# Kernel tuning notes

Measured on AMD Instinct MI355X. Metric: run time of the kernel, lower is better.

## Reference

```python
import jax, jax.numpy as jnp
import numpy as np

V, H, B, S = 32000, 2048, 128, 512
NEG_INF = -1e9

def setup_inputs() -> dict:
    key = jax.random.key(0)
    ks = jax.random.split(key, 12)
    sc = 1.0 / np.sqrt(H)
    embed = jax.random.normal(ks[0], (V, H), jnp.float32) * sc
    embed = embed.at[0].set(0.0)  # padding_idx=0
    return {
        "target_words": jax.random.randint(ks[1], (B,), 0, V),
        "hx": jax.random.normal(ks[2], (B, H), jnp.float32),
        "cx": jax.random.normal(ks[3], (B, H), jnp.float32),
        "ew_hx_list": jax.random.normal(ks[4], (S, B, H), jnp.float32),
        "ew_mask": jax.random.randint(ks[5], (S, B, 1), 0, 2).astype(jnp.int32),
        "embed": embed,
        "W_ih": jax.random.normal(ks[6], (4 * H, H), jnp.float32) * sc,
        "W_hh": jax.random.normal(ks[7], (4 * H, H), jnp.float32) * sc,
        "b_ih": jax.random.normal(ks[8], (4 * H,), jnp.float32) * sc,
        "b_hh": jax.random.normal(ks[9], (4 * H,), jnp.float32) * sc,
        "attn_W": jax.random.normal(ks[10], (H, 2 * H), jnp.float32) * sc,
        "attn_b": jax.random.normal(ks[11], (H,), jnp.float32) * sc,
    }

def reference(target_words, hx, cx, ew_hx_list, ew_mask, embed, W_ih, W_hh, b_ih, b_hh, attn_W, attn_b):
    # forward(): embedding (dropout is identity in eval) + LSTMCell step
    x = embed[target_words]                                   # [B,H]
    gates = x @ W_ih.T + b_ih + hx @ W_hh.T + b_hh            # [B,4H]
    i, f, g, o = jnp.split(gates, 4, axis=-1)                 # PyTorch gate order
    i = jax.nn.sigmoid(i); f = jax.nn.sigmoid(f); o = jax.nn.sigmoid(o)
    g = jnp.tanh(g)
    cx_new = f * cx + i * g
    hx_new = o * jnp.tanh(cx_new)                             # [B,H]
    # attention(): masked dot-score softmax over source dim 0
    scores = jnp.sum(hx_new * ew_hx_list, axis=-1, keepdims=True)  # [S,B,1]
    masked = jnp.where(ew_mask == 0, NEG_INF, scores)
    align = jax.nn.softmax(masked, axis=0)                    # [S,B,1]
    content = jnp.sum(align * ew_hx_list, axis=0)             # [B,H]
    concat = jnp.concatenate([content, hx_new], axis=1)       # [B,2H]
    hx_attention = jnp.tanh(concat @ attn_W.T + attn_b)       # [B,H]
    return hx_attention
```

## Files before the change

kernel.cpp:

```cpp
#include <hip/hip_runtime.h>
#include <math.h>

#define B 128
#define H 2048
#define S 512
#define FOURH 8192

typedef float  f32x4  __attribute__((ext_vector_type(4)));
typedef short  bf16x8 __attribute__((ext_vector_type(8)));
typedef unsigned short u16;
typedef unsigned short u16x8 __attribute__((ext_vector_type(8)));
typedef unsigned short u16x4 __attribute__((ext_vector_type(4)));

__device__ __forceinline__ void cvt_hilo(float x, u16& h, u16& lo) {
    unsigned int u = __float_as_uint(x);
    h = (u16)(u >> 16);
    float hf = __uint_as_float(u & 0xFFFF0000u);
    float r = x - hf;
    lo = (u16)(__float_as_uint(r) >> 16);
}

__global__ __launch_bounds__(256) void gather_convert_A0(
    const int* __restrict__ tw,
    const float* __restrict__ embed,
    const float* __restrict__ hx,
    u16* __restrict__ Ah, u16* __restrict__ Al)
{
    const int i = (blockIdx.x * 256 + threadIdx.x) * 8;
    const int b = i >> 12;
    const int col = i & 4095;
    const float* src = (col < H) ? (embed + (size_t)tw[b] * H + col)
                                 : (hx + (size_t)b * H + (col - H));
    f32x4 v0 = *(const f32x4*)(src);
    f32x4 v1 = *(const f32x4*)(src + 4);
    u16x8 hv, lv;
    #pragma unroll
    for (int j = 0; j < 4; ++j) { u16 h, l; cvt_hilo(v0[j], h, l); hv[j] = h; lv[j] = l; }
    #pragma unroll
    for (int j = 0; j < 4; ++j) { u16 h, l; cvt_hilo(v1[j], h, l); hv[4+j] = h; lv[4+j] = l; }
    *(u16x8*)(Ah + i) = hv;
    *(u16x8*)(Al + i) = lv;
}

template<int MODE>
__global__ __launch_bounds__(256) void split_gemm(
    const u16* __restrict__ Ah, const u16* __restrict__ Al,
    const float* __restrict__ W0, const float* __restrict__ W1,
    float* __restrict__ outp)
{
    constexpr int NOUT = (MODE == 0) ? FOURH : H;
    constexpr int KLEN = (MODE == 0) ? 2048 : 1024;
    __shared__ u16 AhS[128][40];
    __shared__ u16 AlS[128][40];
    __shared__ u16 BhS[32][40];
    __shared__ u16 BlS[32][40];

    const int tid = threadIdx.x;
    const int n0 = blockIdx.x * 32;
    const int kz = blockIdx.y;
    const int kbase = kz * KLEN;
    const int ar = tid >> 1, ac = (tid & 1) * 16;
    const int br = tid >> 3, bc = (tid & 7) * 4;
    const int wv = tid >> 6, lane = tid & 63;
    const int frow = lane & 15, fk = (lane >> 4) * 8, crow = (lane >> 4) * 4;

    const float* Wrow;
    if (MODE == 0)
        Wrow = ((kz == 0) ? W0 : W1) + (size_t)(n0 + br) * H;
    else
        Wrow = W0 + (size_t)(n0 + br) * (2 * H) + kbase;

    const u16* Abase = Ah + (size_t)ar * 4096 + kbase + ac;
    const u16* Lbase = Al + (size_t)ar * 4096 + kbase + ac;

    f32x4 acc[2][2];
    #pragma unroll
    for (int mi = 0; mi < 2; ++mi)
        #pragma unroll
        for (int ni = 0; ni < 2; ++ni)
            acc[mi][ni] = (f32x4){0.f, 0.f, 0.f, 0.f};

    u16x8 rah0, rah1, ral0, ral1;
    f32x4 rbv;
    auto load_tile = [&](int k0) {
        rah0 = *(const u16x8*)(Abase + k0);
        rah1 = *(const u16x8*)(Abase + k0 + 8);
        ral0 = *(const u16x8*)(Lbase + k0);
        ral1 = *(const u16x8*)(Lbase + k0 + 8);
        rbv  = *(const f32x4*)(Wrow + k0 + bc);
    };

    load_tile(0);

    for (int ks = 0; ks < KLEN / 32; ++ks) {
        __syncthreads();
        *(u16x8*)&AhS[ar][ac]     = rah0;
        *(u16x8*)&AhS[ar][ac + 8] = rah1;
        *(u16x8*)&AlS[ar][ac]     = ral0;
        *(u16x8*)&AlS[ar][ac + 8] = ral1;
        u16x4 bh, bl;
        #pragma unroll
        for (int j = 0; j < 4; ++j) { u16 h, l; cvt_hilo(rbv[j], h, l); bh[j] = h; bl[j] = l; }
        *(u16x4*)&BhS[br][bc] = bh;
        *(u16x4*)&BlS[br][bc] = bl;
        __syncthreads();
        if (ks + 1 < KLEN / 32) load_tile((ks + 1) * 32);

        bf16x8 a_h[2], a_l[2], b_h[2], b_l[2];
        #pragma unroll
        for (int mi = 0; mi < 2; ++mi) {
            a_h[mi] = *(const bf16x8*)&AhS[wv * 32 + mi * 16 + frow][fk];
            a_l[mi] = *(const bf16x8*)&AlS[wv * 32 + mi * 16 + frow][fk];
        }
        #pragma unroll
        for (int ni = 0; ni < 2; ++ni) {
            b_h[ni] = *(const bf16x8*)&BhS[ni * 16 + frow][fk];
            b_l[ni] = *(const bf16x8*)&BlS[ni * 16 + frow][fk];
        }
        #pragma unroll
        for (int mi = 0; mi < 2; ++mi)
            #pragma unroll
            for (int ni = 0; ni < 2; ++ni) {
                acc[mi][ni] = __builtin_amdgcn_mfma_f32_16x16x32_bf16(a_h[mi], b_h[ni], acc[mi][ni], 0, 0, 0);
                acc[mi][ni] = __builtin_amdgcn_mfma_f32_16x16x32_bf16(a_h[mi], b_l[ni], acc[mi][ni], 0, 0, 0);
                acc[mi][ni] = __builtin_amdgcn_mfma_f32_16x16x32_bf16(a_l[mi], b_h[ni], acc[mi][ni], 0, 0, 0);
            }
    }

    #pragma unroll
    for (int mi = 0; mi < 2; ++mi)
        #pragma unroll
        for (int ni = 0; ni < 2; ++ni) {
            const int col = n0 + ni * 16 + frow;
            #pragma unroll
            for (int j = 0; j < 4; ++j) {
                const int row = wv * 32 + mi * 16 + crow + j;
                outp[((size_t)kz * B + row) * NOUT + col] = acc[mi][ni][j];
            }
        }
}

__global__ __launch_bounds__(256) void lstm_cell(
    const float* __restrict__ gp,
    const float* __restrict__ cx,
    const float* __restrict__ b_ih,
    const float* __restrict__ b_hh,
    float* __restrict__ hxn,
    u16* __restrict__ Ah1, u16* __restrict__ Al1)
{
    const int t = blockIdx.x * 256 + threadIdx.x;
    const int b = t >> 9;
    const int h = (t & 511) * 4;
    const float* g0 = gp + (size_t)b * FOURH;
    const float* g1 = g0 + (size_t)B * FOURH;
    f32x4 gi = *(const f32x4*)(g0 + h)         + *(const f32x4*)(g1 + h)
             + *(const f32x4*)(b_ih + h)       + *(const f32x4*)(b_hh + h);
    f32x4 gf = *(const f32x4*)(g0 + H + h)     + *(const f32x4*)(g1 + H + h)
             + *(const f32x4*)(b_ih + H + h)   + *(const f32x4*)(b_hh + H + h);
    f32x4 gg = *(const f32x4*)(g0 + 2*H + h)   + *(const f32x4*)(g1 + 2*H + h)
             + *(const f32x4*)(b_ih + 2*H + h) + *(const f32x4*)(b_hh + 2*H + h);
    f32x4 go = *(const f32x4*)(g0 + 3*H + h)   + *(const f32x4*)(g1 + 3*H + h)
             + *(const f32x4*)(b_ih + 3*H + h) + *(const f32x4*)(b_hh + 3*H + h);
    f32x4 cv = *(const f32x4*)(cx + (size_t)b * H + h);
    f32x4 hv;
    #pragma unroll
    for (int j = 0; j < 4; ++j) {
        float i_ = 1.f / (1.f + expf(-gi[j]));
        float f_ = 1.f / (1.f + expf(-gf[j]));
        float o_ = 1.f / (1.f + expf(-go[j]));
        float g_ = tanhf(gg[j]);
        float c_ = f_ * cv[j] + i_ * g_;
        hv[j] = o_ * tanhf(c_);
    }
    *(f32x4*)(hxn + (size_t)b * H + h) = hv;
    u16x4 hh, ll;
    #pragma unroll
    for (int j = 0; j < 4; ++j) { u16 a, l; cvt_hilo(hv[j], a, l); hh[j] = a; ll[j] = l; }
    *(u16x4*)(Ah1 + (size_t)b * 4096 + H + h) = hh;
    *(u16x4*)(Al1 + (size_t)b * 4096 + H + h) = ll;
}

__global__ __launch_bounds__(256) void fused_attn(
    const float* __restrict__ hxn,
    const float* __restrict__ ew,
    const int* __restrict__ mask,
    float* __restrict__ o_part,
    float* __restrict__ ml_part)
{
    __shared__ float mlbuf[4][2];
    __shared__ float obuf[4][2048];

    const int tid = threadIdx.x;
    const int b = blockIdx.x >> 2;
    const int c = blockIdx.x & 3;
    const int wv = tid >> 6;
    const int lane = tid & 63;
    const int s0 = c * 128 + wv * 32;

    unsigned long long mbits;
    {
        int mv = (lane < 32) ? mask[(s0 + lane) * B + b] : 0;
        mbits = __ballot(mv != 0);
    }

    f32x4 hxv[8];
    const float* hp = hxn + (size_t)b * H + lane * 4;
    #pragma unroll
    for (int j = 0; j < 8; ++j) hxv[j] = *(const f32x4*)(hp + j * 256);

    f32x4 o4[8];
    #pragma unroll
    for (int j = 0; j < 8; ++j) o4[j] = (f32x4){0.f, 0.f, 0.f, 0.f};
    float m = -3.0e38f, l = 0.f;

    const size_t SSTRIDE = (size_t)B * H;
    const float* rowp = ew + ((size_t)s0 * B + b) * H + lane * 4;

    f32x4 ev[8];
    #pragma unroll
    for (int j = 0; j < 8; ++j) ev[j] = *(const f32x4*)(rowp + j * 256);

    for (int si = 0; si < 32; ++si) {
        f32x4 cur[8];
        #pragma unroll
        for (int j = 0; j < 8; ++j) cur[j] = ev[j];
        if (si < 31) {
            const float* np = rowp + (size_t)(si + 1) * SSTRIDE;
            #pragma unroll
            for (int j = 0; j < 8; ++j) ev[j] = *(const f32x4*)(np + j * 256);
        }
        float p = 0.f;
        #pragma unroll
        for (int j = 0; j < 8; ++j) {
            f32x4 t = cur[j] * hxv[j];
            p += t[0] + t[1] + t[2] + t[3];
        }
        #pragma unroll
        for (int off = 32; off; off >>= 1) p += __shfl_xor(p, off, 64);
        if (!((mbits >> si) & 1)) p = -1e9f;
        const float mn = fmaxf(m, p);
        const float sc = expf(m - mn);
        const float pe = expf(p - mn);
        l = l * sc + pe;
        #pragma unroll
        for (int j = 0; j < 8; ++j) o4[j] = o4[j] * sc + cur[j] * pe;
        m = mn;
    }

    if (lane == 0) { mlbuf[wv][0] = m; mlbuf[wv][1] = l; }
    __syncthreads();
    const float M = fmaxf(fmaxf(mlbuf[0][0], mlbuf[1][0]), fmaxf(mlbuf[2][0], mlbuf[3][0]));
    const float wsc = expf(m - M);
    float L = 0.f;
    #pragma unroll
    for (int w = 0; w < 4; ++w) L += mlbuf[w][1] * expf(mlbuf[w][0] - M);
    #pragma unroll
    for (int j = 0; j < 8; ++j)
        *(f32x4*)&obuf[wv][j * 256 + lane * 4] = o4[j] * wsc;
    __syncthreads();

    const int h0 = tid * 8;
    f32x4 s0v = (f32x4){0.f, 0.f, 0.f, 0.f}, s1v = s0v;
    #pragma unroll
    for (int w = 0; w < 4; ++w) {
        s0v += *(const f32x4*)&obuf[w][h0];
        s1v += *(const f32x4*)&obuf[w][h0 + 4];
    }
    float* op = o_part + ((size_t)b * 4 + c) * H + h0;
    *(f32x4*)(op)     = s0v;
    *(f32x4*)(op + 4) = s1v;
    if (tid == 0) {
        ml_part[((size_t)b * 4 + c) * 2]     = M;
        ml_part[((size_t)b * 4 + c) * 2 + 1] = L;
    }
}

__global__ __launch_bounds__(256) void attn_combine(
    const float* __restrict__ o_part,
    const float* __restrict__ ml_part,
    u16* __restrict__ Ah1, u16* __restrict__ Al1)
{
    const int b = blockIdx.x;
    const int tid = threadIdx.x;
    float Mc[4], Lc[4];
    #pragma unroll
    for (int c = 0; c < 4; ++c) {
        Mc[c] = ml_part[((size_t)b * 4 + c) * 2];
        Lc[c] = ml_part[((size_t)b * 4 + c) * 2 + 1];
    }
    const float Mg = fmaxf(fmaxf(Mc[0], Mc[1]), fmaxf(Mc[2], Mc[3]));
    float Lg = 0.f;
    #pragma unroll
    for (int c = 0; c < 4; ++c) Lg += Lc[c] * expf(Mc[c] - Mg);
    const float inv = 1.f / Lg;
    const int h0 = tid * 8;
    f32x4 a0 = (f32x4){0.f, 0.f, 0.f, 0.f}, a1 = a0;
    #pragma unroll
    for (int c = 0; c < 4; ++c) {
        const float scl = expf(Mc[c] - Mg) * inv;
        const float* op = o_part + ((size_t)b * 4 + c) * H + h0;
        a0 += *(const f32x4*)(op) * scl;
        a1 += *(const f32x4*)(op + 4) * scl;
    }
    u16x8 hh, ll;
    #pragma unroll
    for (int j = 0; j < 4; ++j) { u16 a, l; cvt_hilo(a0[j], a, l); hh[j] = a; ll[j] = l; }
    #pragma unroll
    for (int j = 0; j < 4; ++j) { u16 a, l; cvt_hilo(a1[j], a, l); hh[4+j] = a; ll[4+j] = l; }
    *(u16x8*)(Ah1 + (size_t)b * 4096 + h0) = hh;
    *(u16x8*)(Al1 + (size_t)b * 4096 + h0) = ll;
}

__global__ __launch_bounds__(256) void attn_out(
    const float* __restrict__ part,
    const float* __restrict__ attn_b,
    float* __restrict__ out)
{
    const int t = blockIdx.x * 256 + threadIdx.x;
    const int i = t * 4;
    const int n = i & (H - 1);
    const size_t BH = (size_t)B * H;
    f32x4 s = *(const f32x4*)(part + i)
            + *(const f32x4*)(part + BH + i)
            + *(const f32x4*)(part + 2 * BH + i)
            + *(const f32x4*)(part + 3 * BH + i)
            + *(const f32x4*)(attn_b + n);
    f32x4 r;
    #pragma unroll
    for (int j = 0; j < 4; ++j) r[j] = tanhf(s[j]);
    *(f32x4*)(out + i) = r;
}

extern "C" void kernel_launch(void* const* d_in, const int* in_sizes, int n_in,
                              void* d_out, int out_size, void* d_ws, size_t ws_size,
                              hipStream_t stream)
{
    const int*   tw     = (const int*)d_in[0];
    const float* hx     = (const float*)d_in[1];
    const float* cx     = (const float*)d_in[2];
    const float* ew     = (const float*)d_in[3];
    const int*   mask   = (const int*)d_in[4];
    const float* embed  = (const float*)d_in[5];
    const float* W_ih   = (const float*)d_in[6];
    const float* W_hh   = (const float*)d_in[7];
    const float* b_ih   = (const float*)d_in[8];
    const float* b_hh   = (const float*)d_in[9];
    const float* attn_W = (const float*)d_in[10];
    const float* attn_b = (const float*)d_in[11];
    float* out = (float*)d_out;

    float* ws      = (float*)d_ws;
    float* gates_p = ws;
    float* o_part  = gates_p + 2 * (size_t)B * FOURH;
    float* ml      = o_part + (size_t)B * 4 * H;
    float* hxn     = ml + 1024;
    float* out_p   = hxn + (size_t)B * H;
    u16* Ah0 = (u16*)(out_p + 4 * (size_t)B * H);
    u16* Al0 = Ah0 + (size_t)B * 4096;
    u16* Ah1 = Al0 + (size_t)B * 4096;
    u16* Al1 = Ah1 + (size_t)B * 4096;

    gather_convert_A0<<<256, 256, 0, stream>>>(tw, embed, hx, Ah0, Al0);
    split_gemm<0><<<dim3(FOURH / 32, 2), 256, 0, stream>>>(Ah0, Al0, W_ih, W_hh, gates_p);
    lstm_cell<<<256, 256, 0, stream>>>(gates_p, cx, b_ih, b_hh, hxn, Ah1, Al1);
    fused_attn<<<B * 4, 256, 0, stream>>>(hxn, ew, mask, o_part, ml);
    attn_combine<<<B, 256, 0, stream>>>(o_part, ml, Ah1, Al1);
    split_gemm<1><<<dim3(H / 32, 4), 256, 0, stream>>>(Ah1, Al1, attn_W, attn_W, out_p);
    attn_out<<<256, 256, 0, stream>>>(out_p, attn_b, out);
}
```

Before: 230.8 us.

## Double split-K factor in both GEMMs and streamline online softmax with exp2

```diff
diff --git a/kernel.cpp b/kernel.cpp
--- a/kernel.cpp
+++ b/kernel.cpp
@@ -5,6 +5,7 @@
 #define H 2048
 #define S 512
 #define FOURH 8192
+#define LOG2E 1.4426950408889634f
 
 typedef float  f32x4  __attribute__((ext_vector_type(4)));
 typedef short  bf16x8 __attribute__((ext_vector_type(8)));
@@ -49,7 +50,7 @@
     float* __restrict__ outp)
 {
     constexpr int NOUT = (MODE == 0) ? FOURH : H;
-    constexpr int KLEN = (MODE == 0) ? 2048 : 1024;
+    constexpr int KLEN = (MODE == 0) ? 1024 : 512;
     __shared__ u16 AhS[128][40];
     __shared__ u16 AlS[128][40];
     __shared__ u16 BhS[32][40];
@@ -66,7 +67,7 @@
 
     const float* Wrow;
     if (MODE == 0)
-        Wrow = ((kz == 0) ? W0 : W1) + (size_t)(n0 + br) * H;
+        Wrow = ((kz < 2) ? W0 : W1) + (size_t)(n0 + br) * H + (kz & 1) * 1024;
     else
         Wrow = W0 + (size_t)(n0 + br) * (2 * H) + kbase;
 
@@ -151,16 +152,19 @@
     const int t = blockIdx.x * 256 + threadIdx.x;
     const int b = t >> 9;
     const int h = (t & 511) * 4;
+    const size_t PS = (size_t)B * FOURH;
     const float* g0 = gp + (size_t)b * FOURH;
-    const float* g1 = g0 + (size_t)B * FOURH;
-    f32x4 gi = *(const f32x4*)(g0 + h)         + *(const f32x4*)(g1 + h)
-             + *(const f32x4*)(b_ih + h)       + *(const f32x4*)(b_hh + h);
-    f32x4 gf = *(const f32x4*)(g0 + H + h)     + *(const f32x4*)(g1 + H + h)
-             + *(const f32x4*)(b_ih + H + h)   + *(const f32x4*)(b_hh + H + h);
-    f32x4 gg = *(const f32x4*)(g0 + 2*H + h)   + *(const f32x4*)(g1 + 2*H + h)
-             + *(const f32x4*)(b_ih + 2*H + h) + *(const f32x4*)(b_hh + 2*H + h);
-    f32x4 go = *(const f32x4*)(g0 + 3*H + h)   + *(const f32x4*)(g1 + 3*H + h)
-             + *(const f32x4*)(b_ih + 3*H + h) + *(const f32x4*)(b_hh + 3*H + h);
+    f32x4 gi = *(const f32x4*)(b_ih + h)       + *(const f32x4*)(b_hh + h);
+    f32x4 gf = *(const f32x4*)(b_ih + H + h)   + *(const f32x4*)(b_hh + H + h);
+    f32x4 gg = *(const f32x4*)(b_ih + 2*H + h) + *(const f32x4*)(b_hh + 2*H + h);
+    f32x4 go = *(const f32x4*)(b_ih + 3*H + h) + *(const f32x4*)(b_hh + 3*H + h);
+    #pragma unroll
+    for (int p = 0; p < 4; ++p) {
+        gi += *(const f32x4*)(g0 + p * PS + h);
+        gf += *(const f32x4*)(g0 + p * PS + H + h);
+        gg += *(const f32x4*)(g0 + p * PS + 2*H + h);
+        go += *(const f32x4*)(g0 + p * PS + 3*H + h);
+    }
     f32x4 cv = *(const f32x4*)(cx + (size_t)b * H + h);
     f32x4 hv;
     #pragma unroll
@@ -211,7 +215,7 @@
     f32x4 o4[8];
     #pragma unroll
     for (int j = 0; j < 8; ++j) o4[j] = (f32x4){0.f, 0.f, 0.f, 0.f};
-    float m = -3.0e38f, l = 0.f;
+    float m2 = -3.0e38f, l = 0.f;
 
     const size_t SSTRIDE = (size_t)B * H;
     const float* rowp = ew + ((size_t)s0 * B + b) * H + lane * 4;
@@ -237,23 +241,28 @@
         }
         #pragma unroll
         for (int off = 32; off; off >>= 1) p += __shfl_xor(p, off, 64);
-        if (!((mbits >> si) & 1)) p = -1e9f;
-        const float mn = fmaxf(m, p);
-        const float sc = expf(m - mn);
-        const float pe = expf(p - mn);
-        l = l * sc + pe;
-        #pragma unroll
-        for (int j = 0; j < 8; ++j) o4[j] = o4[j] * sc + cur[j] * pe;
-        m = mn;
-    }
-
-    if (lane == 0) { mlbuf[wv][0] = m; mlbuf[wv][1] = l; }
+        float p2 = ((mbits >> si) & 1) ? p * LOG2E : -1.5e9f;
+        if (p2 <= m2) {
+            const float pe = exp2f(p2 - m2);
+            l += pe;
+            #pragma unroll
+            for (int j = 0; j < 8; ++j) o4[j] += cur[j] * pe;
+        } else {
+            const float sc = exp2f(m2 - p2);
+            l = l * sc + 1.f;
+            #pragma unroll
+            for (int j = 0; j < 8; ++j) o4[j] = o4[j] * sc + cur[j];
+            m2 = p2;
+        }
+    }
+
+    if (lane == 0) { mlbuf[wv][0] = m2; mlbuf[wv][1] = l; }
     __syncthreads();
     const float M = fmaxf(fmaxf(mlbuf[0][0], mlbuf[1][0]), fmaxf(mlbuf[2][0], mlbuf[3][0]));
-    const float wsc = expf(m - M);
+    const float wsc = exp2f(m2 - M);
     float L = 0.f;
     #pragma unroll
-    for (int w = 0; w < 4; ++w) L += mlbuf[w][1] * expf(mlbuf[w][0] - M);
+    for (int w = 0; w < 4; ++w) L += mlbuf[w][1] * exp2f(mlbuf[w][0] - M);
     #pragma unroll
     for (int j = 0; j < 8; ++j)
         *(f32x4*)&obuf[wv][j * 256 + lane * 4] = o4[j] * wsc;
@@ -291,13 +300,13 @@
     const float Mg = fmaxf(fmaxf(Mc[0], Mc[1]), fmaxf(Mc[2], Mc[3]));
     float Lg = 0.f;
     #pragma unroll
-    for (int c = 0; c < 4; ++c) Lg += Lc[c] * expf(Mc[c] - Mg);
+    for (int c = 0; c < 4; ++c) Lg += Lc[c] * exp2f(Mc[c] - Mg);
     const float inv = 1.f / Lg;
     const int h0 = tid * 8;
     f32x4 a0 = (f32x4){0.f, 0.f, 0.f, 0.f}, a1 = a0;
     #pragma unroll
     for (int c = 0; c < 4; ++c) {
-        const float scl = expf(Mc[c] - Mg) * inv;
+        const float scl = exp2f(Mc[c] - Mg) * inv;
         const float* op = o_part + ((size_t)b * 4 + c) * H + h0;
         a0 += *(const f32x4*)(op) * scl;
         a1 += *(const f32x4*)(op + 4) * scl;
@@ -320,11 +329,9 @@
     const int i = t * 4;
     const int n = i & (H - 1);
     const size_t BH = (size_t)B * H;
-    f32x4 s = *(const f32x4*)(part + i)
-            + *(const f32x4*)(part + BH + i)
-            + *(const f32x4*)(part + 2 * BH + i)
-            + *(const f32x4*)(part + 3 * BH + i)
-            + *(const f32x4*)(attn_b + n);
+    f32x4 s = *(const f32x4*)(attn_b + n);
+    #pragma unroll
+    for (int p = 0; p < 8; ++p) s += *(const f32x4*)(part + p * BH + i);
     f32x4 r;
     #pragma unroll
     for (int j = 0; j < 4; ++j) r[j] = tanhf(s[j]);
@@ -351,20 +358,20 @@
 
     float* ws      = (float*)d_ws;
     float* gates_p = ws;
-    float* o_part  = gates_p + 2 * (size_t)B * FOURH;
+    float* o_part  = gates_p + 4 * (size_t)B * FOURH;
     float* ml      = o_part + (size_t)B * 4 * H;
     float* hxn     = ml + 1024;
     float* out_p   = hxn + (size_t)B * H;
-    u16* Ah0 = (u16*)(out_p + 4 * (size_t)B * H);
+    u16* Ah0 = (u16*)(out_p + 8 * (size_t)B * H);
     u16* Al0 = Ah0 + (size_t)B * 4096;
     u16* Ah1 = Al0 + (size_t)B * 4096;
     u16* Al1 = Ah1 + (size_t)B * 4096;
 
     gather_convert_A0<<<256, 256, 0, stream>>>(tw, embed, hx, Ah0, Al0);
-    split_gemm<0><<<dim3(FOURH / 32, 2), 256, 0, stream>>>(Ah0, Al0, W_ih, W_hh, gates_p);
+    split_gemm<0><<<dim3(FOURH / 32, 4), 256, 0, stream>>>(Ah0, Al0, W_ih, W_hh, gates_p);
     lstm_cell<<<256, 256, 0, stream>>>(gates_p, cx, b_ih, b_hh, hxn, Ah1, Al1);
     fused_attn<<<B * 4, 256, 0, stream>>>(hxn, ew, mask, o_part, ml);
     attn_combine<<<B, 256, 0, stream>>>(o_part, ml, Ah1, Al1);
-    split_gemm<1><<<dim3(H / 32, 4), 256, 0, stream>>>(Ah1, Al1, attn_W, attn_W, out_p);
+    split_gemm<1><<<dim3(H / 32, 8), 256, 0, stream>>>(Ah1, Al1, attn_W, attn_W, out_p);
     attn_out<<<256, 256, 0, stream>>>(out_p, attn_b, out);
 }
```

After: 221.2 us. 4.1% less time.
